# Performance work log

Measured on AMD Instinct MI355X. Metric: run time of the kernel, lower is better.

The kernel has to match this reference:

```python
import jax, jax.numpy as jnp
import numpy as np

jax.config.update("jax_enable_x64", True)  # original casts scores to float64

D_MODEL = 1024
NUM_HEADS = 16
DEPTH = D_MODEL // NUM_HEADS
B = 2
SQK = 1025  # q/k seq len; scores sliced [1:, :-1] -> 1024
SV = 1024   # v / mask seq len


def _split_heads(x, batch):
    # (B, S, D) -> (B, H, S, depth)
    s = x.shape[1]
    return x.reshape(batch, s, NUM_HEADS, DEPTH).transpose(0, 2, 1, 3)


def setup_inputs() -> dict:
    key = jax.random.key(0)
    ks = jax.random.split(key, 12)
    sc = 1.0 / np.sqrt(D_MODEL)
    inp = {
        "v": jax.random.normal(ks[0], (B, SV, D_MODEL), dtype=jnp.float32),
        "k": jax.random.normal(ks[1], (B, SQK, D_MODEL), dtype=jnp.float32),
        "q": jax.random.normal(ks[2], (B, SQK, D_MODEL), dtype=jnp.float32),
        "mask": jax.random.randint(ks[3], (B, SV, SV), 0, 2, dtype=jnp.int32),
        "Wq0": jax.random.normal(ks[4], (D_MODEL, D_MODEL), dtype=jnp.float32) * sc,
        "bq0": jnp.zeros((D_MODEL,), dtype=jnp.float32),
        "Wk0": jax.random.normal(ks[5], (D_MODEL, D_MODEL), dtype=jnp.float32) * sc,
        "bk0": jnp.zeros((D_MODEL,), dtype=jnp.float32),
        "Wv": jax.random.normal(ks[6], (D_MODEL, D_MODEL), dtype=jnp.float32) * sc,
        "bv": jnp.zeros((D_MODEL,), dtype=jnp.float32),
        "Wo": jax.random.normal(ks[7], (D_MODEL, D_MODEL), dtype=jnp.float32) * sc,
        "bo": jnp.zeros((D_MODEL,), dtype=jnp.float32),
    }
    return inp


def reference(v, k, q, mask, Wq0, bq0, Wk0, bk0, Wv, bv, Wo, bo):
    batch = q.shape[0]
    # projections (wq/wk of the original layer are unused in call)
    qq = q @ Wq0 + bq0                      # (B, SQK, D)
    kk = k @ Wk0 + bk0                      # (B, SQK, D)
    vv = v @ Wv + bv                        # (B, SV, D)
    qh = _split_heads(qq, batch)            # (B, H, SQK, depth)
    kh = _split_heads(kk, batch)
    vh = _split_heads(vv, batch)            # (B, H, SV, depth)

    # custom attention: matmul -> slice -> relu/scale -> fp64 -> mask -> softmax
    scores = jnp.einsum("bhqd,bhkd->bhqk", qh, kh)          # (B,H,SQK,SQK)
    scores = scores[:, :, 1:, :-1]                           # (B,H,SV,SV)
    dk = jnp.float64(DEPTH)
    nl = jax.nn.relu(scores / jnp.sqrt(dk)).astype(jnp.float64)
    nl = nl + mask[:, None, :, :].astype(jnp.float64) * (-1e9)
    att_weights = jax.nn.softmax(nl, axis=-1)                # (B,H,SV,SV) fp64

    out = jnp.einsum("bhqk,bhkd->bhqd", att_weights, vh.astype(jnp.float64))
    out = out.transpose(0, 2, 1, 3).reshape(batch, SV, D_MODEL)  # concat heads
    output = out @ Wo.astype(jnp.float64) + bo.astype(jnp.float64)
    return output, att_weights
```

## Files before the change

kernel.cpp:

```cpp
#include <hip/hip_runtime.h>

#define DM   1024
#define NH   16
#define DH   64
#define BATCH 2
#define SEQ  1024
#define QBLK 128
#define KBLK 128

typedef __attribute__((ext_vector_type(8))) short   short8;
typedef __attribute__((ext_vector_type(4))) float   f32x4;
typedef __attribute__((ext_vector_type(4))) unsigned short ushort4v;

__device__ __forceinline__ unsigned short f2bf(float f) {
  unsigned int u = __float_as_uint(f);
  u += 0x7FFFu + ((u >> 16) & 1u);
  return (unsigned short)(u >> 16);
}
__device__ __forceinline__ float bf2f(unsigned short h) {
  return __uint_as_float(((unsigned int)h) << 16);
}
__device__ __forceinline__ void split8(const float4& a, const float4& b,
                                       short8& h, short8& l) {
  float f[8] = {a.x, a.y, a.z, a.w, b.x, b.y, b.z, b.w};
#pragma unroll
  for (int j = 0; j < 8; j++) {
    unsigned short hh = f2bf(f[j]);
    h[j] = (short)hh;
    l[j] = (short)f2bf(f[j] - bf2f(hh));
  }
}

__device__ __forceinline__ void mfma_gemm(
    const float* __restrict__ A, long lda,
    const unsigned short* __restrict__ BTh,
    const unsigned short* __restrict__ BTl, long ldb,
    const float* __restrict__ bias, float* __restrict__ C, long ldc,
    int K, int row0, int col0)
{
  __shared__ short Ah[4][64][8];
  __shared__ short Al[4][64][8];
  __shared__ short Bh[8][64][8];
  __shared__ short Bl[8][64][8];

  const int tid  = threadIdx.x;
  const int wave = tid >> 6, lane = tid & 63;
  const int wm = wave & 1, wn = wave >> 1;

  f32x4 acc[2][4];
#pragma unroll
  for (int i = 0; i < 2; i++)
#pragma unroll
    for (int j = 0; j < 4; j++) acc[i][j] = (f32x4){0.f, 0.f, 0.f, 0.f};

  const int am    = tid >> 2;
  const int ako   = (tid & 3) * 8;
  const int afrag = am >> 4;
  const int alane = (am & 15) + (ako >> 3) * 16;
  const int bn     = tid >> 1;
  const int bkh    = tid & 1;
  const int bfrag  = bn >> 4;
  const int blane0 = (bn & 15) + (bkh * 2) * 16;

  const float*          aptr  = A   + (long)(row0 + am) * lda + ako;
  const unsigned short* bhptr = BTh + (long)(col0 + bn) * ldb + bkh * 16;
  const unsigned short* blptr = BTl + (long)(col0 + bn) * ldb + bkh * 16;

  for (int k0 = 0; k0 < K; k0 += 32) {
    float4 v0 = *(const float4*)(aptr + k0);
    float4 v1 = *(const float4*)(aptr + k0 + 4);
    short8 hv, lv;
    split8(v0, v1, hv, lv);
    *(short8*)&Ah[afrag][alane][0] = hv;
    *(short8*)&Al[afrag][alane][0] = lv;
    short8 b0 = *(const short8*)(bhptr + k0);
    short8 b1 = *(const short8*)(bhptr + k0 + 8);
    short8 c0 = *(const short8*)(blptr + k0);
    short8 c1 = *(const short8*)(blptr + k0 + 8);
    *(short8*)&Bh[bfrag][blane0][0]      = b0;
    *(short8*)&Bh[bfrag][blane0 + 16][0] = b1;
    *(short8*)&Bl[bfrag][blane0][0]      = c0;
    *(short8*)&Bl[bfrag][blane0 + 16][0] = c1;
    __syncthreads();

    short8 a_h[2], a_l[2], b_h[4], b_l[4];
#pragma unroll
    for (int fm = 0; fm < 2; fm++) {
      a_h[fm] = *(short8*)&Ah[wm * 2 + fm][lane][0];
      a_l[fm] = *(short8*)&Al[wm * 2 + fm][lane][0];
    }
#pragma unroll
    for (int fn = 0; fn < 4; fn++) {
      b_h[fn] = *(short8*)&Bh[wn * 4 + fn][lane][0];
      b_l[fn] = *(short8*)&Bl[wn * 4 + fn][lane][0];
    }
#pragma unroll
    for (int fm = 0; fm < 2; fm++)
#pragma unroll
      for (int fn = 0; fn < 4; fn++) {
        acc[fm][fn] = __builtin_amdgcn_mfma_f32_16x16x32_bf16(
            a_h[fm], b_h[fn], acc[fm][fn], 0, 0, 0);
        acc[fm][fn] = __builtin_amdgcn_mfma_f32_16x16x32_bf16(
            a_h[fm], b_l[fn], acc[fm][fn], 0, 0, 0);
        acc[fm][fn] = __builtin_amdgcn_mfma_f32_16x16x32_bf16(
            a_l[fm], b_h[fn], acc[fm][fn], 0, 0, 0);
      }
    __syncthreads();
  }

  const int erow = (lane >> 4) * 4;
  const int ecol = lane & 15;
#pragma unroll
  for (int fm = 0; fm < 2; fm++)
#pragma unroll
    for (int fn = 0; fn < 4; fn++) {
      const int r0 = row0 + wm * 32 + fm * 16 + erow;
      const int cc = col0 + wn * 64 + fn * 16 + ecol;
      const float b = bias ? bias[cc] : 0.f;
#pragma unroll
      for (int i = 0; i < 4; i++)
        C[(long)(r0 + i) * ldc + cc] = acc[fm][fn][i] + b;
    }
}

struct SplitTArgs {
  const float* W[4];
  unsigned short* TH[4];
  unsigned short* TL[4];
};

__global__ __launch_bounds__(256) void splitT_kernel(SplitTArgs s) {
  const int w = blockIdx.z;
  const float* W = s.W[w];
  unsigned short* TH = s.TH[w];
  unsigned short* TL = s.TL[w];
  __shared__ float tile[32][33];
  const int t = threadIdx.x;
  const int k0 = blockIdx.y * 32, n0 = blockIdx.x * 32;
  {
    const int r = t >> 3, c = (t & 7) * 4;
    float4 v = *(const float4*)(W + (long)(k0 + r) * DM + n0 + c);
    tile[r][c] = v.x; tile[r][c + 1] = v.y;
    tile[r][c + 2] = v.z; tile[r][c + 3] = v.w;
  }
  __syncthreads();
  const int n = t >> 3, k = (t & 7) * 4;
  ushort4v h, l;
#pragma unroll
  for (int i = 0; i < 4; i++) {
    float f = tile[k + i][n];
    unsigned short hh = f2bf(f);
    h[i] = hh;
    l[i] = f2bf(f - bf2f(hh));
  }
  *(ushort4v*)(TH + (long)(n0 + n) * DM + k0 + k) = h;
  *(ushort4v*)(TL + (long)(n0 + n) * DM + k0 + k) = l;
}

struct MfmaProjArgs {
  const float* A[3];
  long astride[3];
  const unsigned short* BTh[3];
  const unsigned short* BTl[3];
  const float* bias[3];
  float* C[3];
};

__global__ __launch_bounds__(256) void proj_mfma_kernel(MfmaProjArgs p) {
  const int z = blockIdx.z, sel = z >> 1, b = z & 1;
  const float* A = p.A[sel] + (long)b * p.astride[sel];
  float* C = p.C[sel] + (long)b * SEQ * DM;
  mfma_gemm(A, DM, p.BTh[sel], p.BTl[sel], DM, p.bias[sel], C, DM, DM,
            blockIdx.y * 64, blockIdx.x * 128);
}

__global__ __launch_bounds__(256) void out_mfma_kernel(
    const float* __restrict__ ohs,
    const unsigned short* __restrict__ WoTh,
    const unsigned short* __restrict__ WoTl,
    const float* __restrict__ bo, float* __restrict__ out0) {
  const int b = blockIdx.z;
  mfma_gemm(ohs + (long)b * SEQ * DM, DM, WoTh, WoTl, DM, bo,
            out0 + (long)b * SEQ * DM, DM, DM,
            blockIdx.y * 64, blockIdx.x * 128);
}

__global__ __launch_bounds__(512) void fused_attn_kernel(
    const float* __restrict__ qq, const float* __restrict__ kk,
    const float* __restrict__ vv, const int* __restrict__ mask,
    float* __restrict__ attw, float* __restrict__ ohs)
{
  const int z = blockIdx.y;
  const int b = z >> 4, h = z & 15;
  const int row0 = blockIdx.x * QBLK;

  const float* Q = qq + (long)b * SEQ * DM + h * DH;
  const float* K = kk + (long)b * SEQ * DM + h * DH;
  const float* V = vv + (long)b * SEQ * DM + h * DH;
  const int*  mk = mask + (long)b * SEQ * SEQ;
  float* att  = attw + (long)z * SEQ * SEQ;
  float* ohsb = ohs + (long)b * SEQ * DM + h * DH;

  __shared__ short Kh[8][2][64][8];
  __shared__ short Kl[8][2][64][8];
  __shared__ short Vh[4][4][64][8];
  __shared__ short Vl[4][4][64][8];
  __shared__ float P[8][16][132];

  const int tid  = threadIdx.x;
  const int w    = tid >> 6, lane = tid & 63;
  const int lg   = lane >> 4, lr = lane & 15;
  const int grow = row0 + 16 * w + 4 * lg;

  short8 qh[2], ql[2];
  {
    const float* qp = Q + (long)(row0 + 16 * w + lr) * DM + 8 * lg;
#pragma unroll
    for (int kh = 0; kh < 2; kh++) {
      float4 a = *(const float4*)(qp + 32 * kh);
      float4 bq = *(const float4*)(qp + 32 * kh + 4);
      split8(a, bq, qh[kh], ql[kh]);
    }
  }

  float lsum[4] = {0.f, 0.f, 0.f, 0.f};
  for (int t = 0; t < 8; t++) {
    {
      const int key = tid >> 2, d0 = (tid & 3) * 16;
      const float* kp = K + (long)(t * KBLK + key) * DM + d0;
#pragma unroll
      for (int oct = 0; oct < 2; oct++) {
        const int d = d0 + 8 * oct;
        float4 x = *(const float4*)(kp + 8 * oct);
        float4 y = *(const float4*)(kp + 8 * oct + 4);
        short8 hs;
        float f[8] = {x.x, x.y, x.z, x.w, y.x, y.y, y.z, y.w};
#pragma unroll
        for (int j = 0; j < 8; j++) hs[j] = (short)f2bf(f[j]);
        *(short8*)&Kh[key >> 4][d >> 5][(key & 15) + 16 * ((d & 31) >> 3)][0] = hs;
      }
    }
    __syncthreads();

    f32x4 s[8];
#pragma unroll
    for (int nf = 0; nf < 8; nf++) s[nf] = (f32x4){0.f, 0.f, 0.f, 0.f};
#pragma unroll
    for (int nf = 0; nf < 8; nf++)
#pragma unroll
      for (int kh = 0; kh < 2; kh++) {
        short8 kf = *(short8*)&Kh[nf][kh][lane][0];
        s[nf] = __builtin_amdgcn_mfma_f32_16x16x32_bf16(qh[kh], kf, s[nf], 0, 0, 0);
      }
#pragma unroll
    for (int nf = 0; nf < 8; nf++)
#pragma unroll
      for (int i = 0; i < 4; i++) {
        int m = mk[(long)(grow + i) * SEQ + t * KBLK + 16 * nf + lr];
        float se = fmaxf(s[nf][i] * 0.125f, 0.f) - 1e9f * (float)m;
        lsum[i] += __expf(se);
      }
    __syncthreads();
  }
#pragma unroll
  for (int o = 1; o <= 8; o <<= 1)
#pragma unroll
    for (int i = 0; i < 4; i++)
      lsum[i] += __shfl_xor(lsum[i], o, 64);
  float linv[4];
#pragma unroll
  for (int i = 0; i < 4; i++) linv[i] = 1.f / lsum[i];

  f32x4 o_acc[4];
#pragma unroll
  for (int nf = 0; nf < 4; nf++) o_acc[nf] = (f32x4){0.f, 0.f, 0.f, 0.f};

  for (int t = 0; t < 8; t++) {
    {
      const int key = tid >> 2, d0 = (tid & 3) * 16;
      const float* kp = K + (long)(t * KBLK + key) * DM + d0;
#pragma unroll
      for (int oct = 0; oct < 2; oct++) {
        const int d = d0 + 8 * oct;
        float4 x = *(const float4*)(kp + 8 * oct);
        float4 y = *(const float4*)(kp + 8 * oct + 4);
        short8 hs, ls;
        split8(x, y, hs, ls);
        const int nf2 = key >> 4, kh2 = d >> 5;
        const int ln2 = (key & 15) + 16 * ((d & 31) >> 3);
        *(short8*)&Kh[nf2][kh2][ln2][0] = hs;
        *(short8*)&Kl[nf2][kh2][ln2][0] = ls;
      }
    }
#pragma unroll
    for (int r = 0; r < 4; r++) {
      const int idx = tid + 512 * r;
      const int key = idx >> 4, d0 = (idx & 15) * 4;
      float4 x = *(const float4*)(V + (long)(t * KBLK + key) * DM + d0);
      const int ks = key >> 5, kin = key & 31;
      const int g2 = kin >> 3, j2 = kin & 7;
      float f[4] = {x.x, x.y, x.z, x.w};
#pragma unroll
      for (int i = 0; i < 4; i++) {
        const int d = d0 + i;
        unsigned short hh = f2bf(f[i]);
        Vh[ks][d >> 4][(d & 15) + 16 * g2][j2] = (short)hh;
        Vl[ks][d >> 4][(d & 15) + 16 * g2][j2] = (short)f2bf(f[i] - bf2f(hh));
      }
    }
    __syncthreads();

    f32x4 s[8];
#pragma unroll
    for (int nf = 0; nf < 8; nf++) s[nf] = (f32x4){0.f, 0.f, 0.f, 0.f};
#pragma unroll
    for (int nf = 0; nf < 8; nf++)
#pragma unroll
      for (int kh = 0; kh < 2; kh++) {
        short8 kfh = *(short8*)&Kh[nf][kh][lane][0];
        short8 kfl = *(short8*)&Kl[nf][kh][lane][0];
        s[nf] = __builtin_amdgcn_mfma_f32_16x16x32_bf16(qh[kh], kfh, s[nf], 0, 0, 0);
        s[nf] = __builtin_amdgcn_mfma_f32_16x16x32_bf16(qh[kh], kfl, s[nf], 0, 0, 0);
        s[nf] = __builtin_amdgcn_mfma_f32_16x16x32_bf16(ql[kh], kfh, s[nf], 0, 0, 0);
      }

#pragma unroll
    for (int nf = 0; nf < 8; nf++)
#pragma unroll
      for (int i = 0; i < 4; i++) {
        int m = mk[(long)(grow + i) * SEQ + t * KBLK + 16 * nf + lr];
        float se = fmaxf(s[nf][i] * 0.125f, 0.f) - 1e9f * (float)m;
        P[w][4 * lg + i][16 * nf + lr] = __expf(se) * linv[i];
      }

    short8 pah[4], pal[4];
#pragma unroll
    for (int ks = 0; ks < 4; ks++) {
      float4 x = *(float4*)&P[w][lr][32 * ks + 8 * lg];
      float4 y = *(float4*)&P[w][lr][32 * ks + 8 * lg + 4];
      split8(x, y, pah[ks], pal[ks]);
    }

#pragma unroll
    for (int ks = 0; ks < 4; ks++)
#pragma unroll
      for (int nf = 0; nf < 4; nf++) {
        short8 vfh = *(short8*)&Vh[ks][nf][lane][0];
        short8 vfl = *(short8*)&Vl[ks][nf][lane][0];
        o_acc[nf] = __builtin_amdgcn_mfma_f32_16x16x32_bf16(pah[ks], vfh, o_acc[nf], 0, 0, 0);
        o_acc[nf] = __builtin_amdgcn_mfma_f32_16x16x32_bf16(pah[ks], vfl, o_acc[nf], 0, 0, 0);
        o_acc[nf] = __builtin_amdgcn_mfma_f32_16x16x32_bf16(pal[ks], vfh, o_acc[nf], 0, 0, 0);
      }

#pragma unroll
    for (int rh = 0; rh < 2; rh++)
#pragma unroll
      for (int rr = 0; rr < 4; rr++) {
        const int rl = 8 * rh + (lane >> 3);
        const int c4 = (lane & 7) + 8 * rr;
        float4 pv4 = *(float4*)&P[w][rl][4 * c4];
        *(float4*)(att + (long)(row0 + 16 * w + rl) * SEQ + t * KBLK + 4 * c4) = pv4;
      }
    __syncthreads();
  }

#pragma unroll
  for (int nf = 0; nf < 4; nf++)
#pragma unroll
    for (int i = 0; i < 4; i++)
      ohsb[(long)(grow + i) * DM + 16 * nf + lr] = o_acc[nf][i];
}

extern "C" void kernel_launch(void* const* d_in, const int* in_sizes, int n_in,
                              void* d_out, int out_size, void* d_ws, size_t ws_size,
                              hipStream_t stream)
{
  const float* v    = (const float*)d_in[0];
  const float* k    = (const float*)d_in[1];
  const float* q    = (const float*)d_in[2];
  const int*   mask = (const int*)  d_in[3];
  const float* Wq   = (const float*)d_in[4];
  const float* bq   = (const float*)d_in[5];
  const float* Wk   = (const float*)d_in[6];
  const float* bk   = (const float*)d_in[7];
  const float* Wv   = (const float*)d_in[8];
  const float* bv   = (const float*)d_in[9];
  const float* Wo   = (const float*)d_in[10];
  const float* bo   = (const float*)d_in[11];

  const long NE = (long)SEQ * DM;
  float* qq  = (float*)d_ws;
  float* kkp = qq  + BATCH * NE;
  float* vvp = kkp + BATCH * NE;
  float* ohs = vvp + BATCH * NE;
  unsigned short* WoTh = (unsigned short*)(ohs + BATCH * NE);
  unsigned short* WoTl = WoTh + NE;

  float* out0 = (float*)d_out;
  float* attw = out0 + BATCH * NE;

  unsigned short* stash = (unsigned short*)(attw + (long)BATCH * NH * SEQ * SEQ)
                          - 6L * NE;
  unsigned short* WqTh = stash;
  unsigned short* WqTl = WqTh + NE;
  unsigned short* WkTh = WqTl + NE;
  unsigned short* WkTl = WkTh + NE;
  unsigned short* WvTh = WkTl + NE;
  unsigned short* WvTl = WvTh + NE;

  dim3 blk(256);

  SplitTArgs st;
  st.W[0] = Wq; st.W[1] = Wk; st.W[2] = Wv; st.W[3] = Wo;
  st.TH[0] = WqTh; st.TH[1] = WkTh; st.TH[2] = WvTh; st.TH[3] = WoTh;
  st.TL[0] = WqTl; st.TL[1] = WkTl; st.TL[2] = WvTl; st.TL[3] = WoTl;
  hipLaunchKernelGGL(splitT_kernel, dim3(32, 32, 4), blk, 0, stream, st);

  MfmaProjArgs p;
  p.A[0] = q + DM;  p.A[1] = k;   p.A[2] = v;
  p.astride[0] = 1025L * DM; p.astride[1] = 1025L * DM; p.astride[2] = 1024L * DM;
  p.BTh[0] = WqTh; p.BTh[1] = WkTh; p.BTh[2] = WvTh;
  p.BTl[0] = WqTl; p.BTl[1] = WkTl; p.BTl[2] = WvTl;
  p.bias[0] = bq;  p.bias[1] = bk;  p.bias[2] = bv;
  p.C[0] = qq;     p.C[1] = kkp;    p.C[2] = vvp;
  hipLaunchKernelGGL(proj_mfma_kernel, dim3(8, 16, 6), blk, 0, stream, p);

  hipLaunchKernelGGL(fused_attn_kernel, dim3(SEQ / QBLK, BATCH * NH),
                     dim3(512), 0, stream, qq, kkp, vvp, mask, attw, ohs);

  hipLaunchKernelGGL(out_mfma_kernel, dim3(8, 16, 2), blk, 0, stream,
                     ohs, WoTh, WoTl, bo, out0);
}
```

Baseline: 385.8 us.

## Pre-split activations to bf16 hi/lo, bit-pack mask, halve attention tile

Adds kernels that split the q/k/v inputs into bf16 high/low pairs and pack the int32 mask into bits. The projections now write hi/lo bf16 outputs directly, so the attention and output GEMMs load pre-split operands and skip repeated in-kernel conversion. The attention kernel drops to 64-row query blocks, 256 threads and 64-key tiles, which doubles the block count. It reads mask bits instead of int32 values, cutting mask traffic. The cost is extra launches and extra scratch space carved from the unused tail of the output buffer.

```diff
diff --git a/kernel.cpp b/kernel.cpp
--- a/kernel.cpp
+++ b/kernel.cpp
@@ -5,19 +5,19 @@
 #define DH   64
 #define BATCH 2
 #define SEQ  1024
-#define QBLK 128
-#define KBLK 128
 
 typedef __attribute__((ext_vector_type(8))) short   short8;
 typedef __attribute__((ext_vector_type(4))) float   f32x4;
 typedef __attribute__((ext_vector_type(4))) unsigned short ushort4v;
-
-__device__ __forceinline__ unsigned short f2bf(float f) {
+typedef unsigned short u16;
+typedef unsigned int   u32;
+
+__device__ __forceinline__ u16 f2bf(float f) {
   unsigned int u = __float_as_uint(f);
   u += 0x7FFFu + ((u >> 16) & 1u);
-  return (unsigned short)(u >> 16);
-}
-__device__ __forceinline__ float bf2f(unsigned short h) {
+  return (u16)(u >> 16);
+}
+__device__ __forceinline__ float bf2f(u16 h) {
   return __uint_as_float(((unsigned int)h) << 16);
 }
 __device__ __forceinline__ void split8(const float4& a, const float4& b,
@@ -25,18 +25,19 @@
   float f[8] = {a.x, a.y, a.z, a.w, b.x, b.y, b.z, b.w};
 #pragma unroll
   for (int j = 0; j < 8; j++) {
-    unsigned short hh = f2bf(f[j]);
+    u16 hh = f2bf(f[j]);
     h[j] = (short)hh;
     l[j] = (short)f2bf(f[j] - bf2f(hh));
   }
 }
 
+template<bool SPLIT_OUT>
 __device__ __forceinline__ void mfma_gemm(
-    const float* __restrict__ A, long lda,
-    const unsigned short* __restrict__ BTh,
-    const unsigned short* __restrict__ BTl, long ldb,
-    const float* __restrict__ bias, float* __restrict__ C, long ldc,
-    int K, int row0, int col0)
+    const u16* __restrict__ Ahg, const u16* __restrict__ Alg, long lda,
+    const u16* __restrict__ BTh, const u16* __restrict__ BTl, long ldb,
+    const float* __restrict__ bias,
+    float* __restrict__ Cf, u16* __restrict__ Ch, u16* __restrict__ Cl,
+    long ldc, int K, int row0, int col0)
 {
   __shared__ short Ah[4][64][8];
   __shared__ short Al[4][64][8];
@@ -56,31 +57,24 @@
   const int am    = tid >> 2;
   const int ako   = (tid & 3) * 8;
   const int afrag = am >> 4;
-  const int alane = (am & 15) + (ako >> 3) * 16;
+  const int alane = (am & 15) + 16 * (ako >> 3);
   const int bn     = tid >> 1;
   const int bkh    = tid & 1;
   const int bfrag  = bn >> 4;
-  const int blane0 = (bn & 15) + (bkh * 2) * 16;
-
-  const float*          aptr  = A   + (long)(row0 + am) * lda + ako;
-  const unsigned short* bhptr = BTh + (long)(col0 + bn) * ldb + bkh * 16;
-  const unsigned short* blptr = BTl + (long)(col0 + bn) * ldb + bkh * 16;
+  const int blane0 = (bn & 15) + 32 * bkh;
+
+  const u16* ah = Ahg + (long)(row0 + am) * lda + ako;
+  const u16* al = Alg + (long)(row0 + am) * lda + ako;
+  const u16* bh = BTh + (long)(col0 + bn) * ldb + bkh * 16;
+  const u16* bl = BTl + (long)(col0 + bn) * ldb + bkh * 16;
 
   for (int k0 = 0; k0 < K; k0 += 32) {
-    float4 v0 = *(const float4*)(aptr + k0);
-    float4 v1 = *(const float4*)(aptr + k0 + 4);
-    short8 hv, lv;
-    split8(v0, v1, hv, lv);
-    *(short8*)&Ah[afrag][alane][0] = hv;
-    *(short8*)&Al[afrag][alane][0] = lv;
-    short8 b0 = *(const short8*)(bhptr + k0);
-    short8 b1 = *(const short8*)(bhptr + k0 + 8);
-    short8 c0 = *(const short8*)(blptr + k0);
-    short8 c1 = *(const short8*)(blptr + k0 + 8);
-    *(short8*)&Bh[bfrag][blane0][0]      = b0;
-    *(short8*)&Bh[bfrag][blane0 + 16][0] = b1;
-    *(short8*)&Bl[bfrag][blane0][0]      = c0;
-    *(short8*)&Bl[bfrag][blane0 + 16][0] = c1;
+    *(short8*)&Ah[afrag][alane][0]       = *(const short8*)(ah + k0);
+    *(short8*)&Al[afrag][alane][0]       = *(const short8*)(al + k0);
+    *(short8*)&Bh[bfrag][blane0][0]      = *(const short8*)(bh + k0);
+    *(short8*)&Bh[bfrag][blane0 + 16][0] = *(const short8*)(bh + k0 + 8);
+    *(short8*)&Bl[bfrag][blane0][0]      = *(const short8*)(bl + k0);
+    *(short8*)&Bl[bfrag][blane0 + 16][0] = *(const short8*)(bl + k0 + 8);
     __syncthreads();
 
     short8 a_h[2], a_l[2], b_h[4], b_l[4];
@@ -116,24 +110,33 @@
     for (int fn = 0; fn < 4; fn++) {
       const int r0 = row0 + wm * 32 + fm * 16 + erow;
       const int cc = col0 + wn * 64 + fn * 16 + ecol;
-      const float b = bias ? bias[cc] : 0.f;
-#pragma unroll
-      for (int i = 0; i < 4; i++)
-        C[(long)(r0 + i) * ldc + cc] = acc[fm][fn][i] + b;
+      const float bs = bias ? bias[cc] : 0.f;
+#pragma unroll
+      for (int i = 0; i < 4; i++) {
+        const float val = acc[fm][fn][i] + bs;
+        const long idx = (long)(r0 + i) * ldc + cc;
+        if constexpr (SPLIT_OUT) {
+          u16 hh = f2bf(val);
+          Ch[idx] = hh;
+          Cl[idx] = f2bf(val - bf2f(hh));
+        } else {
+          Cf[idx] = val;
+        }
+      }
     }
 }
 
 struct SplitTArgs {
   const float* W[4];
-  unsigned short* TH[4];
-  unsigned short* TL[4];
+  u16* TH[4];
+  u16* TL[4];
 };
 
 __global__ __launch_bounds__(256) void splitT_kernel(SplitTArgs s) {
   const int w = blockIdx.z;
   const float* W = s.W[w];
-  unsigned short* TH = s.TH[w];
-  unsigned short* TL = s.TL[w];
+  u16* TH = s.TH[w];
+  u16* TL = s.TL[w];
   __shared__ float tile[32][33];
   const int t = threadIdx.x;
   const int k0 = blockIdx.y * 32, n0 = blockIdx.x * 32;
@@ -149,7 +152,7 @@
 #pragma unroll
   for (int i = 0; i < 4; i++) {
     float f = tile[k + i][n];
-    unsigned short hh = f2bf(f);
+    u16 hh = f2bf(f);
     h[i] = hh;
     l[i] = f2bf(f - bf2f(hh));
   }
@@ -157,109 +160,140 @@
   *(ushort4v*)(TL + (long)(n0 + n) * DM + k0 + k) = l;
 }
 
+__global__ __launch_bounds__(256) void input_split_kernel(
+    const float* __restrict__ q, const float* __restrict__ k,
+    const float* __restrict__ v,
+    u16* __restrict__ qh, u16* __restrict__ ql,
+    u16* __restrict__ kh, u16* __restrict__ kl,
+    u16* __restrict__ vh, u16* __restrict__ vl)
+{
+  const int z = blockIdx.z, b = blockIdx.y;
+  const long idx = ((long)blockIdx.x * 256 + threadIdx.x) * 4;
+  const float* src;
+  u16 *dh, *dl;
+  if (z == 0)      { src = q + (long)b * 1025 * DM + DM; dh = qh; dl = ql; }
+  else if (z == 1) { src = k + (long)b * 1025 * DM;      dh = kh; dl = kl; }
+  else             { src = v + (long)b * 1024 * DM;      dh = vh; dl = vl; }
+  float4 x = *(const float4*)(src + idx);
+  ushort4v h, l;
+  float f[4] = {x.x, x.y, x.z, x.w};
+#pragma unroll
+  for (int i = 0; i < 4; i++) {
+    u16 hh = f2bf(f[i]);
+    h[i] = hh;
+    l[i] = f2bf(f[i] - bf2f(hh));
+  }
+  const long o = (long)b * SEQ * DM + idx;
+  *(ushort4v*)(dh + o) = h;
+  *(ushort4v*)(dl + o) = l;
+}
+
+__global__ __launch_bounds__(256) void maskpack_kernel(
+    const int* __restrict__ mask, u32* __restrict__ bits)
+{
+  const long g = (long)blockIdx.x * 256 + threadIdx.x;
+  const int m = mask[g];
+  const unsigned long long bal = __ballot(m != 0);
+  const int lane = threadIdx.x & 63;
+  const long wbase = (g >> 6) << 1;
+  if (lane == 0)  bits[wbase]     = (u32)bal;
+  if (lane == 32) bits[wbase + 1] = (u32)(bal >> 32);
+}
+
 struct MfmaProjArgs {
-  const float* A[3];
-  long astride[3];
-  const unsigned short* BTh[3];
-  const unsigned short* BTl[3];
+  const u16* Ah[3];
+  const u16* Al[3];
+  const u16* BTh[3];
+  const u16* BTl[3];
   const float* bias[3];
-  float* C[3];
+  u16* Ch[3];
+  u16* Cl[3];
 };
 
 __global__ __launch_bounds__(256) void proj_mfma_kernel(MfmaProjArgs p) {
   const int z = blockIdx.z, sel = z >> 1, b = z & 1;
-  const float* A = p.A[sel] + (long)b * p.astride[sel];
-  float* C = p.C[sel] + (long)b * SEQ * DM;
-  mfma_gemm(A, DM, p.BTh[sel], p.BTl[sel], DM, p.bias[sel], C, DM, DM,
-            blockIdx.y * 64, blockIdx.x * 128);
+  const long off = (long)b * SEQ * DM;
+  mfma_gemm<true>(p.Ah[sel] + off, p.Al[sel] + off, DM,
+                  p.BTh[sel], p.BTl[sel], DM, p.bias[sel],
+                  nullptr, p.Ch[sel] + off, p.Cl[sel] + off, DM, DM,
+                  blockIdx.y * 64, blockIdx.x * 128);
 }
 
 __global__ __launch_bounds__(256) void out_mfma_kernel(
-    const float* __restrict__ ohs,
-    const unsigned short* __restrict__ WoTh,
-    const unsigned short* __restrict__ WoTl,
+    const u16* __restrict__ ohsh, const u16* __restrict__ ohsl,
+    const u16* __restrict__ WoTh, const u16* __restrict__ WoTl,
     const float* __restrict__ bo, float* __restrict__ out0) {
   const int b = blockIdx.z;
-  mfma_gemm(ohs + (long)b * SEQ * DM, DM, WoTh, WoTl, DM, bo,
-            out0 + (long)b * SEQ * DM, DM, DM,
-            blockIdx.y * 64, blockIdx.x * 128);
-}
-
-__global__ __launch_bounds__(512) void fused_attn_kernel(
-    const float* __restrict__ qq, const float* __restrict__ kk,
-    const float* __restrict__ vv, const int* __restrict__ mask,
-    float* __restrict__ attw, float* __restrict__ ohs)
+  const long off = (long)b * SEQ * DM;
+  mfma_gemm<false>(ohsh + off, ohsl + off, DM, WoTh, WoTl, DM, bo,
+                   out0 + off, nullptr, nullptr, DM, DM,
+                   blockIdx.y * 64, blockIdx.x * 128);
+}
+
+__global__ __launch_bounds__(256) void fused_attn_kernel(
+    const u16* __restrict__ qqh, const u16* __restrict__ qql,
+    const u16* __restrict__ kkh, const u16* __restrict__ kkl,
+    const u16* __restrict__ vvh, const u16* __restrict__ vvl,
+    const u32* __restrict__ mbits,
+    float* __restrict__ attw, u16* __restrict__ ohsh, u16* __restrict__ ohsl)
 {
-  const int z = blockIdx.y;
-  const int b = z >> 4, h = z & 15;
-  const int row0 = blockIdx.x * QBLK;
-
-  const float* Q = qq + (long)b * SEQ * DM + h * DH;
-  const float* K = kk + (long)b * SEQ * DM + h * DH;
-  const float* V = vv + (long)b * SEQ * DM + h * DH;
-  const int*  mk = mask + (long)b * SEQ * SEQ;
-  float* att  = attw + (long)z * SEQ * SEQ;
-  float* ohsb = ohs + (long)b * SEQ * DM + h * DH;
-
-  __shared__ short Kh[8][2][64][8];
-  __shared__ short Kl[8][2][64][8];
-  __shared__ short Vh[4][4][64][8];
-  __shared__ short Vl[4][4][64][8];
-  __shared__ float P[8][16][132];
-
-  const int tid  = threadIdx.x;
-  const int w    = tid >> 6, lane = tid & 63;
-  const int lg   = lane >> 4, lr = lane & 15;
+  const int z = blockIdx.y, b = z >> 4, h = z & 15;
+  const int row0 = blockIdx.x * 64;
+  const long hoff = (long)b * SEQ * DM + h * DH;
+  float* att = attw + (long)z * SEQ * SEQ;
+  const u32* mrow = mbits + (long)b * SEQ * 32;
+
+  __shared__ short Kh[4][2][64][8];
+  __shared__ short Kl[4][2][64][8];
+  __shared__ short Vh[2][4][64][8];
+  __shared__ short Vl[2][4][64][8];
+  __shared__ float P[4][16][68];
+
+  const int tid = threadIdx.x, w = tid >> 6, lane = tid & 63;
+  const int lg = lane >> 4, lr = lane & 15;
   const int grow = row0 + 16 * w + 4 * lg;
 
-  short8 qh[2], ql[2];
+  short8 qfh[2], qfl[2];
   {
-    const float* qp = Q + (long)(row0 + 16 * w + lr) * DM + 8 * lg;
+    const long qo = hoff + (long)(row0 + 16 * w + lr) * DM + 8 * lg;
 #pragma unroll
     for (int kh = 0; kh < 2; kh++) {
-      float4 a = *(const float4*)(qp + 32 * kh);
-      float4 bq = *(const float4*)(qp + 32 * kh + 4);
-      split8(a, bq, qh[kh], ql[kh]);
+      qfh[kh] = *(const short8*)(qqh + qo + 32 * kh);
+      qfl[kh] = *(const short8*)(qql + qo + 32 * kh);
     }
   }
 
   float lsum[4] = {0.f, 0.f, 0.f, 0.f};
-  for (int t = 0; t < 8; t++) {
-    {
-      const int key = tid >> 2, d0 = (tid & 3) * 16;
-      const float* kp = K + (long)(t * KBLK + key) * DM + d0;
-#pragma unroll
-      for (int oct = 0; oct < 2; oct++) {
-        const int d = d0 + 8 * oct;
-        float4 x = *(const float4*)(kp + 8 * oct);
-        float4 y = *(const float4*)(kp + 8 * oct + 4);
-        short8 hs;
-        float f[8] = {x.x, x.y, x.z, x.w, y.x, y.y, y.z, y.w};
-#pragma unroll
-        for (int j = 0; j < 8; j++) hs[j] = (short)f2bf(f[j]);
-        *(short8*)&Kh[key >> 4][d >> 5][(key & 15) + 16 * ((d & 31) >> 3)][0] = hs;
-      }
-    }
-    __syncthreads();
-
-    f32x4 s[8];
-#pragma unroll
-    for (int nf = 0; nf < 8; nf++) s[nf] = (f32x4){0.f, 0.f, 0.f, 0.f};
-#pragma unroll
-    for (int nf = 0; nf < 8; nf++)
+  for (int t = 0; t < 16; t++) {
+#pragma unroll
+    for (int r = 0; r < 2; r++) {
+      const int c = tid + 256 * r, key = c >> 3, oct = c & 7;
+      *(short8*)&Kh[key >> 4][oct >> 2][(key & 15) + 16 * (oct & 3)][0] =
+          *(const short8*)(kkh + hoff + (long)(t * 64 + key) * DM + 8 * oct);
+    }
+    __syncthreads();
+
+    f32x4 s[4];
+#pragma unroll
+    for (int nf = 0; nf < 4; nf++) s[nf] = (f32x4){0.f, 0.f, 0.f, 0.f};
+#pragma unroll
+    for (int nf = 0; nf < 4; nf++)
 #pragma unroll
       for (int kh = 0; kh < 2; kh++) {
         short8 kf = *(short8*)&Kh[nf][kh][lane][0];
-        s[nf] = __builtin_amdgcn_mfma_f32_16x16x32_bf16(qh[kh], kf, s[nf], 0, 0, 0);
-      }
-#pragma unroll
-    for (int nf = 0; nf < 8; nf++)
-#pragma unroll
-      for (int i = 0; i < 4; i++) {
-        int m = mk[(long)(grow + i) * SEQ + t * KBLK + 16 * nf + lr];
-        float se = fmaxf(s[nf][i] * 0.125f, 0.f) - 1e9f * (float)m;
-        lsum[i] += __expf(se);
-      }
+        s[nf] = __builtin_amdgcn_mfma_f32_16x16x32_bf16(qfh[kh], kf, s[nf], 0, 0, 0);
+      }
+#pragma unroll
+    for (int i = 0; i < 4; i++) {
+      const uint2 mw = *(const uint2*)(mrow + (long)(grow + i) * 32 + t * 2);
+      const u32 w0 = mw.x >> lr, w1 = mw.y >> lr;
+#pragma unroll
+      for (int nf = 0; nf < 4; nf++) {
+        const u32 bit = (((nf & 2) ? w1 : w0) >> ((nf & 1) << 4)) & 1u;
+        const float e = __expf(fmaxf(s[nf][i] * 0.125f, 0.f));
+        lsum[i] += bit ? 0.f : e;
+      }
+    }
     __syncthreads();
   }
 #pragma unroll
@@ -275,74 +309,68 @@
 #pragma unroll
   for (int nf = 0; nf < 4; nf++) o_acc[nf] = (f32x4){0.f, 0.f, 0.f, 0.f};
 
-  for (int t = 0; t < 8; t++) {
-    {
-      const int key = tid >> 2, d0 = (tid & 3) * 16;
-      const float* kp = K + (long)(t * KBLK + key) * DM + d0;
-#pragma unroll
-      for (int oct = 0; oct < 2; oct++) {
-        const int d = d0 + 8 * oct;
-        float4 x = *(const float4*)(kp + 8 * oct);
-        float4 y = *(const float4*)(kp + 8 * oct + 4);
-        short8 hs, ls;
-        split8(x, y, hs, ls);
-        const int nf2 = key >> 4, kh2 = d >> 5;
-        const int ln2 = (key & 15) + 16 * ((d & 31) >> 3);
-        *(short8*)&Kh[nf2][kh2][ln2][0] = hs;
-        *(short8*)&Kl[nf2][kh2][ln2][0] = ls;
-      }
-    }
-#pragma unroll
-    for (int r = 0; r < 4; r++) {
-      const int idx = tid + 512 * r;
-      const int key = idx >> 4, d0 = (idx & 15) * 4;
-      float4 x = *(const float4*)(V + (long)(t * KBLK + key) * DM + d0);
-      const int ks = key >> 5, kin = key & 31;
-      const int g2 = kin >> 3, j2 = kin & 7;
-      float f[4] = {x.x, x.y, x.z, x.w};
-#pragma unroll
-      for (int i = 0; i < 4; i++) {
-        const int d = d0 + i;
-        unsigned short hh = f2bf(f[i]);
-        Vh[ks][d >> 4][(d & 15) + 16 * g2][j2] = (short)hh;
-        Vl[ks][d >> 4][(d & 15) + 16 * g2][j2] = (short)f2bf(f[i] - bf2f(hh));
-      }
-    }
-    __syncthreads();
-
-    f32x4 s[8];
-#pragma unroll
-    for (int nf = 0; nf < 8; nf++) s[nf] = (f32x4){0.f, 0.f, 0.f, 0.f};
-#pragma unroll
-    for (int nf = 0; nf < 8; nf++)
+  for (int t = 0; t < 16; t++) {
+#pragma unroll
+    for (int r = 0; r < 2; r++) {
+      const int c = tid + 256 * r, key = c >> 3, oct = c & 7;
+      const long gk = hoff + (long)(t * 64 + key) * DM + 8 * oct;
+      const int nf = key >> 4, khf = oct >> 2;
+      const int ln = (key & 15) + 16 * (oct & 3);
+      *(short8*)&Kh[nf][khf][ln][0] = *(const short8*)(kkh + gk);
+      *(short8*)&Kl[nf][khf][ln][0] = *(const short8*)(kkl + gk);
+    }
+#pragma unroll
+    for (int r = 0; r < 2; r++) {
+      const int c = tid + 256 * r, key = c >> 3, oct = c & 7, d0 = oct * 8;
+      const long gv = hoff + (long)(t * 64 + key) * DM + d0;
+      short8 vh8 = *(const short8*)(vvh + gv);
+      short8 vl8 = *(const short8*)(vvl + gv);
+      const int ks = key >> 5, g2 = (key & 31) >> 3, j = key & 7;
+#pragma unroll
+      for (int e = 0; e < 8; e++) {
+        const int d = d0 + e;
+        Vh[ks][d >> 4][(d & 15) + 16 * g2][j] = vh8[e];
+        Vl[ks][d >> 4][(d & 15) + 16 * g2][j] = vl8[e];
+      }
+    }
+    __syncthreads();
+
+    f32x4 s[4];
+#pragma unroll
+    for (int nf = 0; nf < 4; nf++) s[nf] = (f32x4){0.f, 0.f, 0.f, 0.f};
+#pragma unroll
+    for (int nf = 0; nf < 4; nf++)
 #pragma unroll
       for (int kh = 0; kh < 2; kh++) {
         short8 kfh = *(short8*)&Kh[nf][kh][lane][0];
         short8 kfl = *(short8*)&Kl[nf][kh][lane][0];
-        s[nf] = __builtin_amdgcn_mfma_f32_16x16x32_bf16(qh[kh], kfh, s[nf], 0, 0, 0);
-        s[nf] = __builtin_amdgcn_mfma_f32_16x16x32_bf16(qh[kh], kfl, s[nf], 0, 0, 0);
-        s[nf] = __builtin_amdgcn_mfma_f32_16x16x32_bf16(ql[kh], kfh, s[nf], 0, 0, 0);
-      }
-
-#pragma unroll
-    for (int nf = 0; nf < 8; nf++)
-#pragma unroll
-      for (int i = 0; i < 4; i++) {
-        int m = mk[(long)(grow + i) * SEQ + t * KBLK + 16 * nf + lr];
-        float se = fmaxf(s[nf][i] * 0.125f, 0.f) - 1e9f * (float)m;
-        P[w][4 * lg + i][16 * nf + lr] = __expf(se) * linv[i];
-      }
-
-    short8 pah[4], pal[4];
-#pragma unroll
-    for (int ks = 0; ks < 4; ks++) {
+        s[nf] = __builtin_amdgcn_mfma_f32_16x16x32_bf16(qfh[kh], kfh, s[nf], 0, 0, 0);
+        s[nf] = __builtin_amdgcn_mfma_f32_16x16x32_bf16(qfh[kh], kfl, s[nf], 0, 0, 0);
+        s[nf] = __builtin_amdgcn_mfma_f32_16x16x32_bf16(qfl[kh], kfh, s[nf], 0, 0, 0);
+      }
+
+#pragma unroll
+    for (int i = 0; i < 4; i++) {
+      const uint2 mw = *(const uint2*)(mrow + (long)(grow + i) * 32 + t * 2);
+      const u32 w0 = mw.x >> lr, w1 = mw.y >> lr;
+#pragma unroll
+      for (int nf = 0; nf < 4; nf++) {
+        const u32 bit = (((nf & 2) ? w1 : w0) >> ((nf & 1) << 4)) & 1u;
+        const float e = __expf(fmaxf(s[nf][i] * 0.125f, 0.f)) * linv[i];
+        P[w][4 * lg + i][16 * nf + lr] = bit ? 0.f : e;
+      }
+    }
+
+    short8 pah[2], pal[2];
+#pragma unroll
+    for (int ks = 0; ks < 2; ks++) {
       float4 x = *(float4*)&P[w][lr][32 * ks + 8 * lg];
       float4 y = *(float4*)&P[w][lr][32 * ks + 8 * lg + 4];
       split8(x, y, pah[ks], pal[ks]);
     }
 
 #pragma unroll
-    for (int ks = 0; ks < 4; ks++)
+    for (int ks = 0; ks < 2; ks++)
 #pragma unroll
       for (int nf = 0; nf < 4; nf++) {
         short8 vfh = *(short8*)&Vh[ks][nf][lane][0];
@@ -353,22 +381,24 @@
       }
 
 #pragma unroll
-    for (int rh = 0; rh < 2; rh++)
-#pragma unroll
-      for (int rr = 0; rr < 4; rr++) {
-        const int rl = 8 * rh + (lane >> 3);
-        const int c4 = (lane & 7) + 8 * rr;
-        float4 pv4 = *(float4*)&P[w][rl][4 * c4];
-        *(float4*)(att + (long)(row0 + 16 * w + rl) * SEQ + t * KBLK + 4 * c4) = pv4;
-      }
+    for (int rr = 0; rr < 4; rr++) {
+      const int row = (lane >> 4) + 4 * rr;
+      float4 pv = *(float4*)&P[w][row][4 * (lane & 15)];
+      *(float4*)(att + (long)(row0 + 16 * w + row) * SEQ + t * 64 + 4 * (lane & 15)) = pv;
+    }
     __syncthreads();
   }
 
 #pragma unroll
   for (int nf = 0; nf < 4; nf++)
 #pragma unroll
-    for (int i = 0; i < 4; i++)
-      ohsb[(long)(grow + i) * DM + 16 * nf + lr] = o_acc[nf][i];
+    for (int i = 0; i < 4; i++) {
+      const float o = o_acc[nf][i];
+      const u16 hh = f2bf(o);
+      const long idx = (long)b * SEQ * DM + (long)(grow + i) * DM + h * DH + 16 * nf + lr;
+      ohsh[idx] = hh;
+      ohsl[idx] = f2bf(o - bf2f(hh));
+    }
 }
 
 extern "C" void kernel_launch(void* const* d_in, const int* in_sizes, int n_in,
@@ -388,25 +418,37 @@
   const float* Wo   = (const float*)d_in[10];
   const float* bo   = (const float*)d_in[11];
 
-  const long NE = (long)SEQ * DM;
-  float* qq  = (float*)d_ws;
-  float* kkp = qq  + BATCH * NE;
-  float* vvp = kkp + BATCH * NE;
-  float* ohs = vvp + BATCH * NE;
-  unsigned short* WoTh = (unsigned short*)(ohs + BATCH * NE);
-  unsigned short* WoTl = WoTh + NE;
+  const long NE  = (long)SEQ * DM;
+  const long BNE = (long)BATCH * NE;
+
+  u16* qqh  = (u16*)d_ws;
+  u16* qql  = qqh  + BNE;
+  u16* kkh  = qql  + BNE;
+  u16* kkl  = kkh  + BNE;
+  u16* vvh  = kkl  + BNE;
+  u16* vvl  = vvh  + BNE;
+  u16* ohsh = vvl  + BNE;
+  u16* ohsl = ohsh + BNE;
+  u16* WoTh = ohsl + BNE;
+  u16* WoTl = WoTh + NE;
+  u32* mbits = (u32*)(WoTl + NE);
 
   float* out0 = (float*)d_out;
-  float* attw = out0 + BATCH * NE;
-
-  unsigned short* stash = (unsigned short*)(attw + (long)BATCH * NH * SEQ * SEQ)
-                          - 6L * NE;
-  unsigned short* WqTh = stash;
-  unsigned short* WqTl = WqTh + NE;
-  unsigned short* WkTh = WqTl + NE;
-  unsigned short* WkTl = WkTh + NE;
-  unsigned short* WvTh = WkTl + NE;
-  unsigned short* WvTl = WvTh + NE;
+  float* attw = out0 + BNE;
+
+  u16* sbase = (u16*)(attw + (long)BATCH * NH * SEQ * SEQ) - 18L * NE;
+  u16* WqTh = sbase;
+  u16* WqTl = WqTh + NE;
+  u16* WkTh = WqTl + NE;
+  u16* WkTl = WkTh + NE;
+  u16* WvTh = WkTl + NE;
+  u16* WvTl = WvTh + NE;
+  u16* qinh = WvTl + NE;
+  u16* qinl = qinh + BNE;
+  u16* kinh = qinl + BNE;
+  u16* kinl = kinh + BNE;
+  u16* vinh = kinl + BNE;
+  u16* vinl = vinh + BNE;
 
   dim3 blk(256);
 
@@ -416,18 +458,27 @@
   st.TL[0] = WqTl; st.TL[1] = WkTl; st.TL[2] = WvTl; st.TL[3] = WoTl;
   hipLaunchKernelGGL(splitT_kernel, dim3(32, 32, 4), blk, 0, stream, st);
 
+  hipLaunchKernelGGL(input_split_kernel, dim3(1024, BATCH, 3), blk, 0, stream,
+                     q, k, v, qinh, qinl, kinh, kinl, vinh, vinl);
+
+  hipLaunchKernelGGL(maskpack_kernel, dim3(8192), blk, 0, stream, mask, mbits);
+
   MfmaProjArgs p;
-  p.A[0] = q + DM;  p.A[1] = k;   p.A[2] = v;
-  p.astride[0] = 1025L * DM; p.astride[1] = 1025L * DM; p.astride[2] = 1024L * DM;
-  p.BTh[0] = WqTh; p.BTh[1] = WkTh; p.BTh[2] = WvTh;
-  p.BTl[0] = WqTl; p.BTl[1] = WkTl; p.BTl[2] = WvTl;
-  p.bias[0] = bq;  p.bias[1] = bk;  p.bias[2] = bv;
-  p.C[0] = qq;     p.C[1] = kkp;    p.C[2] = vvp;
+  p.Ah[0] = qinh; p.Al[0] = qinl;
+  p.Ah[1] = kinh; p.Al[1] = kinl;
+  p.Ah[2] = vinh; p.Al[2] = vinl;
+  p.BTh[0] = WqTh; p.BTl[0] = WqTl;
+  p.BTh[1] = WkTh; p.BTl[1] = WkTl;
+  p.BTh[2] = WvTh; p.BTl[2] = WvTl;
+  p.bias[0] = bq; p.bias[1] = bk; p.bias[2] = bv;
+  p.Ch[0] = qqh; p.Cl[0] = qql;
+  p.Ch[1] = kkh; p.Cl[1] = kkl;
+  p.Ch[2] = vvh; p.Cl[2] = vvl;
   hipLaunchKernelGGL(proj_mfma_kernel, dim3(8, 16, 6), blk, 0, stream, p);
 
-  hipLaunchKernelGGL(fused_attn_kernel, dim3(SEQ / QBLK, BATCH * NH),
-                     dim3(512), 0, stream, qq, kkp, vvp, mask, attw, ohs);
+  hipLaunchKernelGGL(fused_attn_kernel, dim3(16, BATCH * NH), blk, 0, stream,
+                     qqh, qql, kkh, kkl, vvh, vvl, mbits, attw, ohsh, ohsl);
 
   hipLaunchKernelGGL(out_mfma_kernel, dim3(8, 16, 2), blk, 0, stream,
-                     ohs, WoTh, WoTl, bo, out0);
-}
+                     ohsh, ohsl, WoTh, WoTl, bo, out0);
+}
```

New measurement: 385.2 us. No clear change (-0.2%).
